# Performance work log

Hardware: AMD Instinct MI355X
Metric: run time of the kernel (lower is better)

The kernel has to match this reference:

```python
import jax, jax.numpy as jnp
import numpy as np

B, C, H, W = 4, 256, 64, 64
N = H * W


def setup_inputs() -> dict:
    key = jax.random.key(0)
    k1, k2, k3, k4, k5 = jax.random.split(key, 5)
    energy = jax.random.normal(k1, (B, N, N), dtype=jnp.float32)
    x = jax.random.normal(k2, (B, C, H, W), dtype=jnp.float32)
    # 1x1 conv params (kernel is [C_out, C_in] after squeezing the 1x1 spatial dims)
    fan = 1.0 / np.sqrt(C)
    value_w = jax.random.uniform(k3, (C, C), dtype=jnp.float32, minval=-fan, maxval=fan)
    value_b = jax.random.uniform(k4, (C,), dtype=jnp.float32, minval=-fan, maxval=fan)
    # nn.Parameter(torch.zeros(1)) -> use small random scalar so output is non-trivial
    gamma = jax.random.normal(k5, (1,), dtype=jnp.float32) * 0.1
    return {"energy": energy, "x": x, "value_w": value_w, "value_b": value_b, "gamma": gamma}


def reference(energy, x, value_w, value_b, gamma):
    # softmax over last dim of the [B, N, N] score matrix (dropout in eval mode = identity)
    attention = jax.nn.softmax(energy, axis=-1)  # [B, N, N]
    # 1x1 conv: per-pixel channel mixing
    value = jnp.einsum('bchw,oc->bohw', x, value_w) + value_b[None, :, None, None]
    value = value.reshape(x.shape[0], -1, N)  # [B, C, N]
    # out[b,c,m] = sum_n value[b,c,n] * attention[b,m,n]  (bmm with attention^T)
    out = jnp.einsum('bcn,bmn->bcm', value, attention)
    out = out.reshape(x.shape)  # [B, C, H, W]
    return gamma[0] * out + 2.0 * x
```

## Files before the change

kernel.cpp:

```cpp
#include <hip/hip_runtime.h>

#define Nn 4096
#define Cc 256
#define NN2 ((size_t)Nn * Nn)

typedef __attribute__((ext_vector_type(8))) short bf16x8;
typedef __attribute__((ext_vector_type(4))) float f32x4;

__device__ __forceinline__ unsigned short f2bf(float f) {
    union { float f; unsigned u; } v; v.f = f;
    unsigned r = v.u + 0x7FFF + ((v.u >> 16) & 1);
    return (unsigned short)(r >> 16);
}

__device__ __forceinline__ bf16x8 pack2(const float4& a, const float4& b) {
    bf16x8 o;
    o[0] = (short)f2bf(a.x); o[1] = (short)f2bf(a.y);
    o[2] = (short)f2bf(a.z); o[3] = (short)f2bf(a.w);
    o[4] = (short)f2bf(b.x); o[5] = (short)f2bf(b.y);
    o[6] = (short)f2bf(b.z); o[7] = (short)f2bf(b.w);
    return o;
}

__device__ __forceinline__ void expstore(const float4& a, const float4& b,
                                         unsigned short* dst, float& sacc) {
    const float s0 = __expf(a.x), s1 = __expf(a.y), s2 = __expf(a.z), s3 = __expf(a.w);
    const float s4 = __expf(b.x), s5 = __expf(b.y), s6 = __expf(b.z), s7 = __expf(b.w);
    sacc += ((s0 + s1) + (s2 + s3)) + ((s4 + s5) + (s6 + s7));
    bf16x8 o;
    o[0] = (short)f2bf(s0); o[1] = (short)f2bf(s1);
    o[2] = (short)f2bf(s2); o[3] = (short)f2bf(s3);
    o[4] = (short)f2bf(s4); o[5] = (short)f2bf(s5);
    o[6] = (short)f2bf(s6); o[7] = (short)f2bf(s7);
    *(bf16x8*)dst = o;
}

__global__ __launch_bounds__(256) void value_gemm(
    const float* __restrict__ X, const float* __restrict__ W,
    const float* __restrict__ bias, unsigned short* __restrict__ Vout)
{
    const int t = threadIdx.x;
    const int b  = blockIdx.x >> 7;
    const int n0 = (blockIdx.x & 127) << 5;
    const int wave = t >> 6, lane = t & 63;
    const int lrow = lane & 15, lq = lane >> 4;

    const float* Xb = X + (size_t)b * Cc * Nn;
    f32x4 acc[4][2] = {};

    #pragma unroll 2
    for (int k0 = 0; k0 < Cc; k0 += 32) {
        bf16x8 af[4];
        #pragma unroll
        for (int ci = 0; ci < 4; ++ci) {
            const float* wp = W + (size_t)(wave * 64 + ci * 16 + lrow) * Cc + k0 + lq * 8;
            af[ci] = pack2(*(const float4*)wp, *(const float4*)(wp + 4));
        }
        bf16x8 bp[2];
        #pragma unroll
        for (int mi = 0; mi < 2; ++mi) {
            const int n = n0 + mi * 16 + lrow;
            const float* xp = Xb + (size_t)(k0 + lq * 8) * Nn + n;
            bf16x8 o;
            #pragma unroll
            for (int j = 0; j < 8; ++j) o[j] = (short)f2bf(xp[(size_t)j * Nn]);
            bp[mi] = o;
        }
        #pragma unroll
        for (int ci = 0; ci < 4; ++ci)
            #pragma unroll
            for (int mi = 0; mi < 2; ++mi)
                acc[ci][mi] = __builtin_amdgcn_mfma_f32_16x16x32_bf16(
                    af[ci], bp[mi], acc[ci][mi], 0, 0, 0);
    }

    #pragma unroll
    for (int ci = 0; ci < 4; ++ci) {
        #pragma unroll
        for (int rr = 0; rr < 4; ++rr) {
            const int o = wave * 64 + ci * 16 + lq * 4 + rr;
            const float bo = bias[o];
            #pragma unroll
            for (int mi = 0; mi < 2; ++mi) {
                const int n = n0 + mi * 16 + lrow;
                Vout[((size_t)(b * Cc + o)) * Nn + n] = f2bf(acc[ci][mi][rr] + bo);
            }
        }
    }
}

__global__ __launch_bounds__(512) void attn_gemm(
    const unsigned short* __restrict__ V, const float* __restrict__ E,
    const float* __restrict__ X, const float* __restrict__ gamma,
    float* __restrict__ Out)
{
    __shared__ unsigned short Bbuf[2][64 * 64];
    __shared__ float sum_lds[64];

    const int t = threadIdx.x;
    const int blk = blockIdx.x;
    const int b  = blk & 3;
    const int m0 = (blk >> 2) << 6;

    const int wave = t >> 6, lane = t & 63;
    const int wm = wave >> 1, wn = wave & 1;
    const int lrow = lane & 15, lq = lane >> 4;
    const int l7 = lrow & 7;

    const int erow = t >> 3, eg = t & 7;
    const float* ep = E + (size_t)b * NN2 + (size_t)(m0 + erow) * Nn + eg * 8;
    unsigned short* const bst0 = &Bbuf[0][erow * 64 + ((eg ^ (erow & 7)) << 3)];
    unsigned short* const bst1 = &Bbuf[1][erow * 64 + ((eg ^ (erow & 7)) << 3)];

    const unsigned short* vbase = V + (size_t)(b * Cc + wm * 64) * Nn;
    int voff[4];
    #pragma unroll
    for (int ci = 0; ci < 4; ++ci) voff[ci] = (ci * 16 + lrow) * Nn + lq * 8;

    f32x4 acc[4][2] = {};
    float sacc = 0.f;

    float4 eA0, eA1, eB0, eB1;
    bf16x8 vA[8], vB[8];

    eA0 = *(const float4*)(ep);        eA1 = *(const float4*)(ep + 4);
    eB0 = *(const float4*)(ep + 64);   eB1 = *(const float4*)(ep + 68);
    #pragma unroll
    for (int kk = 0; kk < 2; ++kk)
        #pragma unroll
        for (int ci = 0; ci < 4; ++ci)
            vA[kk * 4 + ci] = *(const bf16x8*)(vbase + voff[ci] + kk * 32);
    expstore(eA0, eA1, bst0, sacc);
    eA0 = *(const float4*)(ep + 128);  eA1 = *(const float4*)(ep + 132);
    __syncthreads();

    for (int k = 0; k < 64; k += 2) {
        {
            bf16x8 bfr[2][2];
            #pragma unroll
            for (int kk = 0; kk < 2; ++kk)
                #pragma unroll
                for (int mi = 0; mi < 2; ++mi) {
                    const int rm = wn * 32 + mi * 16 + lrow;
                    bfr[kk][mi] = *(const bf16x8*)&Bbuf[0][rm * 64 + (((kk * 4 + lq) ^ l7) << 3)];
                }
            const int kv = (k + 1) << 6;
            #pragma unroll
            for (int kk = 0; kk < 2; ++kk)
                #pragma unroll
                for (int ci = 0; ci < 4; ++ci)
                    vB[kk * 4 + ci] = *(const bf16x8*)(vbase + voff[ci] + kv + kk * 32);
            expstore(eB0, eB1, bst1, sacc);
            const int ke = ((k + 3) & 63) << 6;
            eB0 = *(const float4*)(ep + ke); eB1 = *(const float4*)(ep + ke + 4);
            #pragma unroll
            for (int ci = 0; ci < 4; ++ci)
                #pragma unroll
                for (int mi = 0; mi < 2; ++mi)
                    #pragma unroll
                    for (int kk = 0; kk < 2; ++kk)
                        acc[ci][mi] = __builtin_amdgcn_mfma_f32_16x16x32_bf16(
                            vA[kk * 4 + ci], bfr[kk][mi], acc[ci][mi], 0, 0, 0);
            __syncthreads();
        }
        {
            bf16x8 bfr[2][2];
            #pragma unroll
            for (int kk = 0; kk < 2; ++kk)
                #pragma unroll
                for (int mi = 0; mi < 2; ++mi) {
                    const int rm = wn * 32 + mi * 16 + lrow;
                    bfr[kk][mi] = *(const bf16x8*)&Bbuf[1][rm * 64 + (((kk * 4 + lq) ^ l7) << 3)];
                }
            const int kv = ((k + 2) & 63) << 6;
            #pragma unroll
            for (int kk = 0; kk < 2; ++kk)
                #pragma unroll
                for (int ci = 0; ci < 4; ++ci)
                    vA[kk * 4 + ci] = *(const bf16x8*)(vbase + voff[ci] + kv + kk * 32);
            if (k != 62) {
                expstore(eA0, eA1, bst0, sacc);
                const int ke = ((k + 4) & 63) << 6;
                eA0 = *(const float4*)(ep + ke); eA1 = *(const float4*)(ep + ke + 4);
            }
            #pragma unroll
            for (int ci = 0; ci < 4; ++ci)
                #pragma unroll
                for (int mi = 0; mi < 2; ++mi)
                    #pragma unroll
                    for (int kk = 0; kk < 2; ++kk)
                        acc[ci][mi] = __builtin_amdgcn_mfma_f32_16x16x32_bf16(
                            vB[kk * 4 + ci], bfr[kk][mi], acc[ci][mi], 0, 0, 0);
            __syncthreads();
        }
    }

    {
        float s = sacc;
        s += __shfl_xor(s, 1);
        s += __shfl_xor(s, 2);
        s += __shfl_xor(s, 4);
        if (eg == 0) sum_lds[erow] = s;
    }
    __syncthreads();

    const float g = gamma[0];
    #pragma unroll
    for (int mi = 0; mi < 2; ++mi) {
        const int mloc = wn * 32 + mi * 16 + lrow;
        const float scale = g / sum_lds[mloc];
        const int m = m0 + mloc;
        #pragma unroll
        for (int ci = 0; ci < 4; ++ci) {
            #pragma unroll
            for (int rr = 0; rr < 4; ++rr) {
                const int c = wm * 64 + ci * 16 + lq * 4 + rr;
                const size_t off = ((size_t)(b * Cc + c)) * Nn + m;
                Out[off] = scale * acc[ci][mi][rr] + 2.0f * X[off];
            }
        }
    }
}

extern "C" void kernel_launch(void* const* d_in, const int* in_sizes, int n_in,
                              void* d_out, int out_size, void* d_ws, size_t ws_size,
                              hipStream_t stream) {
    const float* energy  = (const float*)d_in[0];
    const float* x       = (const float*)d_in[1];
    const float* value_w = (const float*)d_in[2];
    const float* value_b = (const float*)d_in[3];
    const float* gamma   = (const float*)d_in[4];
    float* out = (float*)d_out;
    unsigned short* Vws = (unsigned short*)d_ws;

    value_gemm<<<512, 256, 0, stream>>>(x, value_w, value_b, Vws);
    attn_gemm<<<256, 512, 0, stream>>>(Vws, energy, x, gamma, out);
}
```

Before: 450.7 us.

## Stage X tile in LDS for value GEMM and relax attention barriers

The value GEMM now loads its 256x32 slice of X into shared memory with coalesced float4 reads, replacing the strided per-element global loads. In the attention GEMM, __syncthreads is replaced by a barrier that waits only on LDS counters, so outstanding global prefetches of energy and V are not drained at each step. The MFMA blocks are also wrapped in s_setprio raises. The combined aim is better memory coalescing and more overlap of loads with compute. The risk is that relying on lgkmcnt alone depends on the global loads not feeding LDS before the barrier.

```diff
diff --git a/kernel.cpp b/kernel.cpp
--- a/kernel.cpp
+++ b/kernel.cpp
@@ -6,6 +6,11 @@
 
 typedef __attribute__((ext_vector_type(8))) short bf16x8;
 typedef __attribute__((ext_vector_type(4))) float f32x4;
+
+#define LDSBAR() do { \
+    asm volatile("s_waitcnt lgkmcnt(0)" ::: "memory"); \
+    __builtin_amdgcn_s_barrier(); \
+} while (0)
 
 __device__ __forceinline__ unsigned short f2bf(float f) {
     union { float f; unsigned u; } v; v.f = f;
@@ -39,13 +44,28 @@
     const float* __restrict__ X, const float* __restrict__ W,
     const float* __restrict__ bias, unsigned short* __restrict__ Vout)
 {
+    __shared__ float Xs[256][33];
+
     const int t = threadIdx.x;
     const int b  = blockIdx.x >> 7;
     const int n0 = (blockIdx.x & 127) << 5;
     const int wave = t >> 6, lane = t & 63;
     const int lrow = lane & 15, lq = lane >> 4;
 
-    const float* Xb = X + (size_t)b * Cc * Nn;
+    const float* Xb = X + (size_t)b * Cc * Nn + n0;
+
+    {
+        const int r0 = t >> 3, c4 = (t & 7) << 2;
+        #pragma unroll
+        for (int i = 0; i < 8; ++i) {
+            const int r = r0 + i * 32;
+            const float4 v = *(const float4*)(Xb + (size_t)r * Nn + c4);
+            Xs[r][c4 + 0] = v.x; Xs[r][c4 + 1] = v.y;
+            Xs[r][c4 + 2] = v.z; Xs[r][c4 + 3] = v.w;
+        }
+    }
+    __syncthreads();
+
     f32x4 acc[4][2] = {};
 
     #pragma unroll 2
@@ -59,11 +79,10 @@
         bf16x8 bp[2];
         #pragma unroll
         for (int mi = 0; mi < 2; ++mi) {
-            const int n = n0 + mi * 16 + lrow;
-            const float* xp = Xb + (size_t)(k0 + lq * 8) * Nn + n;
+            const int n = mi * 16 + lrow;
             bf16x8 o;
             #pragma unroll
-            for (int j = 0; j < 8; ++j) o[j] = (short)f2bf(xp[(size_t)j * Nn]);
+            for (int j = 0; j < 8; ++j) o[j] = (short)f2bf(Xs[k0 + lq * 8 + j][n]);
             bp[mi] = o;
         }
         #pragma unroll
@@ -132,7 +151,7 @@
             vA[kk * 4 + ci] = *(const bf16x8*)(vbase + voff[ci] + kk * 32);
     expstore(eA0, eA1, bst0, sacc);
     eA0 = *(const float4*)(ep + 128);  eA1 = *(const float4*)(ep + 132);
-    __syncthreads();
+    LDSBAR();
 
     for (int k = 0; k < 64; k += 2) {
         {
@@ -153,6 +172,7 @@
             expstore(eB0, eB1, bst1, sacc);
             const int ke = ((k + 3) & 63) << 6;
             eB0 = *(const float4*)(ep + ke); eB1 = *(const float4*)(ep + ke + 4);
+            __builtin_amdgcn_s_setprio(1);
             #pragma unroll
             for (int ci = 0; ci < 4; ++ci)
                 #pragma unroll
@@ -161,7 +181,8 @@
                     for (int kk = 0; kk < 2; ++kk)
                         acc[ci][mi] = __builtin_amdgcn_mfma_f32_16x16x32_bf16(
                             vA[kk * 4 + ci], bfr[kk][mi], acc[ci][mi], 0, 0, 0);
-            __syncthreads();
+            __builtin_amdgcn_s_setprio(0);
+            LDSBAR();
         }
         {
             bf16x8 bfr[2][2];
@@ -183,6 +204,7 @@
                 const int ke = ((k + 4) & 63) << 6;
                 eA0 = *(const float4*)(ep + ke); eA1 = *(const float4*)(ep + ke + 4);
             }
+            __builtin_amdgcn_s_setprio(1);
             #pragma unroll
             for (int ci = 0; ci < 4; ++ci)
                 #pragma unroll
@@ -191,7 +213,8 @@
                     for (int kk = 0; kk < 2; ++kk)
                         acc[ci][mi] = __builtin_amdgcn_mfma_f32_16x16x32_bf16(
                             vB[kk * 4 + ci], bfr[kk][mi], acc[ci][mi], 0, 0, 0);
-            __syncthreads();
+            __builtin_amdgcn_s_setprio(0);
+            LDSBAR();
         }
     }
 
@@ -202,7 +225,7 @@
         s += __shfl_xor(s, 4);
         if (eg == 0) sum_lds[erow] = s;
     }
-    __syncthreads();
+    LDSBAR();
 
     const float g = gamma[0];
     #pragma unroll
```

Result: no change. 451.3 us (+0.1%).
